# Kernel tuning notes

Measured on AMD Instinct MI355X. Metric: run time of the kernel, lower is better.

## Reference

```python
import jax, jax.numpy as jnp
import numpy as np

NUM_HEADS = 8

def setup_inputs() -> dict:
    key = jax.random.key(0)
    ks = jax.random.split(key, 8)
    B, T, J, N, C = 4, 16, 17, 17, 256
    x = jax.random.normal(ks[0], (B, T, J, N, C), dtype=jnp.float32)
    A_s = jax.random.uniform(ks[1], (J, J), dtype=jnp.float32)
    A_v = jax.random.uniform(ks[2], (N, N), dtype=jnp.float32)
    W_qkv = jax.random.normal(ks[3], (C, 5 * C), dtype=jnp.float32) * (C ** -0.5)
    W_proj = jax.random.normal(ks[4], (3 * C, C), dtype=jnp.float32) * ((3 * C) ** -0.5)
    b_proj = jnp.zeros((C,), dtype=jnp.float32)
    # M ~ xavier_uniform(gain=1.414) over shape (1, J, N, C)
    bound = 1.414 * np.sqrt(6.0 / (N + C))
    M = jax.random.uniform(ks[5], (1, J, N, C), dtype=jnp.float32, minval=-bound, maxval=bound)
    adj_s = jnp.full((J, J), 1e-6, dtype=jnp.float32)  # torch stores (1,1,J,J); broadcast-identical
    adj_v = jnp.full((N, N), 1e-6, dtype=jnp.float32)
    return {"x": x, "A_s": A_s, "A_v": A_v, "W_qkv": W_qkv, "W_proj": W_proj,
            "b_proj": b_proj, "M": M, "adj_s": adj_s, "adj_v": adj_v}


def reference(x, A_s, A_v, W_qkv, W_proj, b_proj, M, adj_s, adj_v):
    B, T, J, N, C = x.shape
    h = NUM_HEADS
    hc = C // h
    scale = hc ** -0.5
    bt = B * T
    xr = x.reshape(bt, J, N, C)
    # qkv Linear (no bias) then view(..., C, 5): channel-interleaved split
    qkv = (xr @ W_qkv).reshape(bt, J, N, C, 5)
    q, k, vs, vv, vsv = (qkv[..., i] * M for i in range(5))
    def heads(t):
        return t.reshape(bt, J, N, h, hc)
    q, k, vs, vv, vsv = map(heads, (q, k, vs, vv, vsv))
    # spatial attention over joints j (per node n), temporal/variate attention over n (per j)
    att_s_o = jnp.einsum('bjnhc,bknhc->bhnjk', q, k) * scale   # (bt,h,N,J,J)
    att_v_o = jnp.einsum('bjnhc,bjmhc->bhjnm', q, k) * scale   # (bt,h,J,N,N)
    att_s = jax.nn.softmax(att_s_o, axis=-1)
    att_v = jax.nn.softmax(att_v_o, axis=-1)
    # outer-product combine, algebraically separated:
    # x_vsv[b,j,n,:] = sum_{k,m} att_s[b,h,n,j,k] * att_v[b,h,j,n,m] * vsv[b,k,m,h,:]
    r = jnp.einsum('bhjnm,bkmhc->bhjnkc', att_v, vsv)           # (bt,h,J,N,J,hc)
    x_vsv = jnp.einsum('bhnjk,bhjnkc->bjnhc', att_s, r).reshape(bt, J, N, C)
    # adjacency-biased attentions (symmetrized learned bias + fixed adjacency)
    adjs = A_s + adj_s
    adjs = (adjs.T + adjs) * 0.5
    adjv = A_v + adj_v
    adjv = (adjv.T + adjv) * 0.5
    att_s2 = jax.nn.softmax(att_s_o + adjs, axis=-1)
    att_v2 = jax.nn.softmax(att_v_o + adjv, axis=-1)
    x_vs = jnp.einsum('bhnjk,bknhc->bjnhc', att_s2, vs).reshape(bt, J, N, C)
    x_vv = jnp.einsum('bhjnm,bjmhc->bjnhc', att_v2, vv).reshape(bt, J, N, C)
    out = jnp.concatenate([x_vsv, x_vs, x_vv], axis=-1) @ W_proj + b_proj
    return out.reshape(B, T, J, N, C)
```

## Files before the change

kernel.cpp:

```cpp
#include <hip/hip_runtime.h>
#include <math.h>

#define ROWS 18496
#define SCALE 0.17677669529663687f

typedef unsigned short ushort_t;
typedef __attribute__((ext_vector_type(8))) short short8;
typedef __attribute__((ext_vector_type(4))) float f32x4;

__device__ __forceinline__ void fma4(float4& d, float s, const float4& v) {
    d.x = fmaf(s, v.x, d.x); d.y = fmaf(s, v.y, d.y);
    d.z = fmaf(s, v.z, d.z); d.w = fmaf(s, v.w, d.w);
}
__device__ __forceinline__ float dot4(const float4& a, const float4& b) {
    return a.x*b.x + a.y*b.y + a.z*b.z + a.w*b.w;
}

__device__ __forceinline__ ushort_t f2bf(float x) {
    union { float f; unsigned u; } v; v.f = x;
    unsigned r = v.u + 0x7fffu + ((v.u >> 16) & 1u);
    return (ushort_t)(r >> 16);
}
__device__ __forceinline__ float bf2f(ushort_t b) {
    union { unsigned u; float f; } v; v.u = ((unsigned)b) << 16; return v.f;
}

__device__ __forceinline__ void gl_lds16(const void* g, void* l) {
    __builtin_amdgcn_global_load_lds(
        (const __attribute__((address_space(1))) void*)g,
        (__attribute__((address_space(3))) void*)l, 16, 0, 0);
}

__device__ __forceinline__ void store_hilo(ushort_t* yhi, ushort_t* ylo,
                                           size_t off, const float4& a)
{
    ushort4 h, l;
    h.x = f2bf(a.x); l.x = f2bf(a.x - bf2f(h.x));
    h.y = f2bf(a.y); l.y = f2bf(a.y - bf2f(h.y));
    h.z = f2bf(a.z); l.z = f2bf(a.z - bf2f(h.z));
    h.w = f2bf(a.w); l.w = f2bf(a.w - bf2f(h.w));
    *(ushort4*)&yhi[off] = h;
    *(ushort4*)&ylo[off] = l;
}

__global__ __launch_bounds__(256) void k_cvt_xw(
    const float4* __restrict__ x, ushort4* __restrict__ xhi, ushort4* __restrict__ xlo,
    const float* __restrict__ W, ushort_t* __restrict__ bh, ushort_t* __restrict__ bl)
{
    if (blockIdx.x < 4624) {
        int i = blockIdx.x * 256 + threadIdx.x;
        float4 v = x[i];
        ushort4 h, l;
        h.x = f2bf(v.x); l.x = f2bf(v.x - bf2f(h.x));
        h.y = f2bf(v.y); l.y = f2bf(v.y - bf2f(h.y));
        h.z = f2bf(v.z); l.z = f2bf(v.z - bf2f(h.z));
        h.w = f2bf(v.w); l.w = f2bf(v.w - bf2f(h.w));
        xhi[i] = h; xlo[i] = l;
    } else {
        int o = blockIdx.x - 4624;
        int kk = threadIdx.x;
        int col = (o & 255) * 5 + (o >> 8);
        float v = W[(size_t)kk * 1280 + col];
        ushort_t hh = f2bf(v);
        bh[(size_t)o * 256 + kk] = hh;
        bl[(size_t)o * 256 + kk] = f2bf(v - bf2f(hh));
    }
}

__global__ __launch_bounds__(256) void k_cvt_wp(
    const float* __restrict__ W, ushort_t* __restrict__ bh, ushort_t* __restrict__ bl)
{
    int n = blockIdx.x;
    for (int k = threadIdx.x; k < 768; k += 256) {
        float v = W[(size_t)k * 256 + n];
        ushort_t h = f2bf(v);
        bh[(size_t)n * 768 + k] = h;
        bl[(size_t)n * 768 + k] = f2bf(v - bf2f(h));
    }
}

template<int BM, int BN, int K, int MODE>
__global__ __launch_bounds__(256) void k_gemm(
    const ushort_t* __restrict__ Ahi, const ushort_t* __restrict__ Alo,
    const ushort_t* __restrict__ Bhi, const ushort_t* __restrict__ Blo,
    const float* __restrict__ aux,
    float* __restrict__ out)
{
    constexpr int MT = BM / 32;
    constexpr int NT = BN / 32;
    __shared__ __attribute__((aligned(16))) ushort_t sAh[BM * 32];
    __shared__ __attribute__((aligned(16))) ushort_t sAl[BM * 32];
    __shared__ __attribute__((aligned(16))) ushort_t sBh[BN * 32];
    __shared__ __attribute__((aligned(16))) ushort_t sBl[BN * 32];

    const int t = threadIdx.x;
    const int lane = t & 63;
    const int ln = lane & 15, quad = lane >> 4;
    const int wave = t >> 6;
    const int wm = wave >> 1, wn = wave & 1;
    const int m0 = blockIdx.y * BM, n0 = blockIdx.x * BN;

    f32x4 acc[MT][NT];
#pragma unroll
    for (int i = 0; i < MT; ++i)
#pragma unroll
        for (int j = 0; j < NT; ++j) acc[i][j] = (f32x4){0.f, 0.f, 0.f, 0.f};

    for (int kb = 0; kb < K; kb += 32) {
        __syncthreads();
#pragma unroll
        for (int s = t; s < BM * 4; s += 256) {
            int row = s >> 2, kc = s & 3;
            int gr = m0 + row; if (gr > ROWS - 1) gr = ROWS - 1;
            size_t gb = ((size_t)gr * K + kb) * 2 + kc * 16;
            int lb = (s & ~63) * 16;
            gl_lds16((const char*)Ahi + gb, (char*)sAh + lb);
            gl_lds16((const char*)Alo + gb, (char*)sAl + lb);
        }
#pragma unroll
        for (int s = t; s < BN * 4; s += 256) {
            int row = s >> 2, kc = s & 3;
            size_t gb = ((size_t)(n0 + row) * K + kb) * 2 + kc * 16;
            int lb = (s & ~63) * 16;
            gl_lds16((const char*)Bhi + gb, (char*)sBh + lb);
            gl_lds16((const char*)Blo + gb, (char*)sBl + lb);
        }
        __syncthreads();

        short8 ah[MT], al[MT], bh[NT], bl[NT];
#pragma unroll
        for (int i = 0; i < MT; ++i) {
            int off = (wm * (BM / 2) + i * 16 + ln) * 32 + quad * 8;
            ah[i] = *(const short8*)&sAh[off];
            al[i] = *(const short8*)&sAl[off];
        }
#pragma unroll
        for (int j = 0; j < NT; ++j) {
            int off = (wn * (BN / 2) + j * 16 + ln) * 32 + quad * 8;
            bh[j] = *(const short8*)&sBh[off];
            bl[j] = *(const short8*)&sBl[off];
        }
#pragma unroll
        for (int i = 0; i < MT; ++i)
#pragma unroll
            for (int j = 0; j < NT; ++j) {
                acc[i][j] = __builtin_amdgcn_mfma_f32_16x16x32_bf16(ah[i], bh[j], acc[i][j], 0, 0, 0);
                acc[i][j] = __builtin_amdgcn_mfma_f32_16x16x32_bf16(ah[i], bl[j], acc[i][j], 0, 0, 0);
                acc[i][j] = __builtin_amdgcn_mfma_f32_16x16x32_bf16(al[i], bh[j], acc[i][j], 0, 0, 0);
            }
    }

#pragma unroll
    for (int i = 0; i < MT; ++i) {
#pragma unroll
        for (int r = 0; r < 4; ++r) {
            int gm = m0 + wm * (BM / 2) + i * 16 + quad * 4 + r;
            if (gm >= ROWS) continue;
            if (MODE == 0) {
                int jn = gm % 289;
                const float* Mrow = &aux[(size_t)jn * 256];
#pragma unroll
                for (int j = 0; j < NT; ++j) {
                    int gn = n0 + wn * (BN / 2) + j * 16 + ln;
                    out[(size_t)gm * 1280 + gn] = acc[i][j][r] * Mrow[gn & 255];
                }
            } else {
#pragma unroll
                for (int j = 0; j < NT; ++j) {
                    int gn = n0 + wn * (BN / 2) + j * 16 + ln;
                    out[(size_t)gm * 256 + gn] = acc[i][j][r] + aux[gn];
                }
            }
        }
    }
}

__global__ __launch_bounds__(512) void k_att(
    const float* __restrict__ qkv5,
    const float* __restrict__ A_s, const float* __restrict__ A_v,
    const float* __restrict__ adjS, const float* __restrict__ adjV,
    ushort_t* __restrict__ yhi, ushort_t* __restrict__ ylo)
{
    __shared__ __attribute__((aligned(16))) float sm[16184];
    float* aS  = sm;
    float* aV  = sm + 4913;
    float* ebS = sm + 9826;
    float* ebV = sm + 10115;
    float* buf = sm + 10404;

    const int t  = threadIdx.x;
    const int bh = blockIdx.x;
    const int b  = bh >> 3, h = bh & 7;
    const size_t rowbase = (size_t)b * 289;

    for (int idx = t; idx < 578; idx += 512) {
        int f = idx / 289, rem = idx % 289;
        int jj = rem / 17, kk = rem % 17;
        float bias;
        if (f == 0)
            bias = 0.5f * ((A_s[jj*17+kk] + adjS[jj*17+kk]) + (A_s[kk*17+jj] + adjS[kk*17+jj]));
        else
            bias = 0.5f * ((A_v[jj*17+kk] + adjV[jj*17+kk]) + (A_v[kk*17+jj] + adjV[kk*17+jj]));
        (f ? ebV : ebS)[rem] = expf(bias);
    }

    float accA[17], accB[17];
#pragma unroll
    for (int i = 0; i < 17; ++i) { accA[i] = 0.f; accB[i] = 0.f; }
    const int u2 = t + 512;
    for (int ch = 0; ch < 2; ++ch) {
        __syncthreads();
        for (int idx = t; idx < 1156; idx += 512) {
            int p = idx >> 2, c = idx & 3;
            *(float4*)&buf[p * 20 + c * 4] =
                *(const float4*)&qkv5[(rowbase + p) * 1280 + 256 + h * 32 + ch * 16 + c * 4];
        }
        __syncthreads();
        {
            const bool isS = (t < 289);
            const int p = isS ? t : t - 289;
            const float* qp = &qkv5[(rowbase + p) * 1280 + h * 32 + ch * 16];
            float4 q0 = *(const float4*)&qp[0];
            float4 q1 = *(const float4*)&qp[4];
            float4 q2 = *(const float4*)&qp[8];
            float4 q3 = *(const float4*)&qp[12];
            const int a = p / 17, bb = p % 17;
            if (isS) {
#pragma unroll
                for (int kk = 0; kk < 17; ++kk) {
                    const float4* r = (const float4*)&buf[(kk * 17 + bb) * 20];
                    accA[kk] += dot4(q0, r[0]) + dot4(q1, r[1]) + dot4(q2, r[2]) + dot4(q3, r[3]);
                }
            } else {
#pragma unroll
                for (int mm = 0; mm < 17; ++mm) {
                    const float4* r = (const float4*)&buf[(a * 17 + mm) * 20];
                    accA[mm] += dot4(q0, r[0]) + dot4(q1, r[1]) + dot4(q2, r[2]) + dot4(q3, r[3]);
                }
            }
        }
        if (u2 < 578) {
            const int p = u2 - 289;
            const float* qp = &qkv5[(rowbase + p) * 1280 + h * 32 + ch * 16];
            float4 q0 = *(const float4*)&qp[0];
            float4 q1 = *(const float4*)&qp[4];
            float4 q2 = *(const float4*)&qp[8];
            float4 q3 = *(const float4*)&qp[12];
            const int a = p / 17;
#pragma unroll
            for (int mm = 0; mm < 17; ++mm) {
                const float4* r = (const float4*)&buf[(a * 17 + mm) * 20];
                accB[mm] += dot4(q0, r[0]) + dot4(q1, r[1]) + dot4(q2, r[2]) + dot4(q3, r[3]);
            }
        }
    }
    {
        if (t < 289) {
            const int a = t / 17, bb = t % 17;
#pragma unroll
            for (int kk = 0; kk < 17; ++kk) aS[bb * 289 + a * 17 + kk] = accA[kk] * SCALE;
        } else {
            const int p = t - 289;
            const int a = p / 17, bb = p % 17;
#pragma unroll
            for (int mm = 0; mm < 17; ++mm) aV[a * 289 + bb * 17 + mm] = accA[mm] * SCALE;
        }
        if (u2 < 578) {
            const int p = u2 - 289;
            const int a = p / 17, bb = p % 17;
#pragma unroll
            for (int mm = 0; mm < 17; ++mm) aV[a * 289 + bb * 17 + mm] = accB[mm] * SCALE;
        }
    }
    __syncthreads();

    for (int idx = t; idx < 578; idx += 512) {
        float* row = (idx < 289) ? &aS[idx * 17] : &aV[(idx - 289) * 17];
        float v[17];
#pragma unroll
        for (int kk = 0; kk < 17; ++kk) v[kk] = row[kk];
        float mx = v[0];
#pragma unroll
        for (int kk = 1; kk < 17; ++kk) mx = fmaxf(mx, v[kk]);
        float sum = 0.f;
#pragma unroll
        for (int kk = 0; kk < 17; ++kk) { v[kk] = expf(v[kk] - mx); sum += v[kk]; }
        float inv = 1.f / sum;
#pragma unroll
        for (int kk = 0; kk < 17; ++kk) row[kk] = v[kk] * inv;
    }

    for (int ch = 0; ch < 2; ++ch) {
        __syncthreads();
        for (int idx = t; idx < 1156; idx += 512) {
            int p = idx >> 2, c = idx & 3;
            *(float4*)&buf[p * 20 + c * 4] =
                *(const float4*)&qkv5[(rowbase + p) * 1280 + 1024 + h * 32 + ch * 16 + c * 4];
        }
        __syncthreads();
        for (int u = t; u < 580; u += 512) {
            const int c4 = (u & 3) * 4;
            const int pb = (u >> 2) * 2;
            const int nv = (289 - pb < 2) ? 1 : 2;
            const int p1 = (pb + 1 > 288) ? 288 : pb + 1;
            const int jj0 = pb / 17, nn0 = pb % 17;
            const int jj1 = p1 / 17, nn1 = p1 % 17;
            float eV0[17], eV1[17];
            {
                const float* s0 = &aV[jj0 * 289 + nn0 * 17];
                const float* s1 = &aV[jj1 * 289 + nn1 * 17];
#pragma unroll
                for (int m = 0; m < 17; ++m) { eV0[m] = s0[m]; eV1[m] = s1[m]; }
            }
            float4 acc0 = {0,0,0,0}, acc1 = {0,0,0,0};
            for (int kk = 0; kk < 17; ++kk) {
                float4 tg0 = {0,0,0,0}, tg1 = {0,0,0,0};
#pragma unroll
                for (int m = 0; m < 17; ++m) {
                    float4 v = *(const float4*)&buf[(kk * 17 + m) * 20 + c4];
                    fma4(tg0, eV0[m], v);
                    fma4(tg1, eV1[m], v);
                }
                fma4(acc0, aS[nn0 * 289 + jj0 * 17 + kk], tg0);
                fma4(acc1, aS[nn1 * 289 + jj1 * 17 + kk], tg1);
            }
            store_hilo(yhi, ylo, (rowbase + pb) * 768 + h * 32 + ch * 16 + c4, acc0);
            if (nv == 2)
                store_hilo(yhi, ylo, (rowbase + pb + 1) * 768 + h * 32 + ch * 16 + c4, acc1);
        }
    }

    for (int ch = 0; ch < 2; ++ch) {
        __syncthreads();
        for (int idx = t; idx < 1156; idx += 512) {
            int p = idx >> 2, c = idx & 3;
            *(float4*)&buf[p * 20 + c * 4] =
                *(const float4*)&qkv5[(rowbase + p) * 1280 + 512 + h * 32 + ch * 16 + c * 4];
        }
        __syncthreads();
        for (int u = t; u < 1156; u += 512) {
            const int c4 = (u & 3) * 4, rest = u >> 2;
            const int n = rest % 17, j = rest / 17;
            float w[17];
            float s = 0.f;
            const float* as = &aS[n * 289 + j * 17];
            const float* eb = &ebS[j * 17];
#pragma unroll
            for (int kk = 0; kk < 17; ++kk) { w[kk] = as[kk] * eb[kk]; s += w[kk]; }
            const float inv = 1.f / s;
            float4 a0 = {0,0,0,0};
            for (int kk = 0; kk < 17; ++kk) {
                float4 v = *(const float4*)&buf[(kk * 17 + n) * 20 + c4];
                fma4(a0, w[kk], v);
            }
            a0.x *= inv; a0.y *= inv; a0.z *= inv; a0.w *= inv;
            store_hilo(yhi, ylo, (rowbase + j * 17 + n) * 768 + 256 + h * 32 + ch * 16 + c4, a0);
        }
    }

    for (int ch = 0; ch < 2; ++ch) {
        __syncthreads();
        for (int idx = t; idx < 1156; idx += 512) {
            int p = idx >> 2, c = idx & 3;
            *(float4*)&buf[p * 20 + c * 4] =
                *(const float4*)&qkv5[(rowbase + p) * 1280 + 768 + h * 32 + ch * 16 + c * 4];
        }
        __syncthreads();
        for (int u = t; u < 1156; u += 512) {
            const int c4 = (u & 3) * 4, rest = u >> 2;
            const int j = rest % 17, n = rest / 17;
            float w[17];
            float s = 0.f;
            const float* av = &aV[j * 289 + n * 17];
            const float* eb = &ebV[n * 17];
#pragma unroll
            for (int mm = 0; mm < 17; ++mm) { w[mm] = av[mm] * eb[mm]; s += w[mm]; }
            const float inv = 1.f / s;
            float4 a0 = {0,0,0,0};
            for (int mm = 0; mm < 17; ++mm) {
                float4 v = *(const float4*)&buf[(j * 17 + mm) * 20 + c4];
                fma4(a0, w[mm], v);
            }
            a0.x *= inv; a0.y *= inv; a0.z *= inv; a0.w *= inv;
            store_hilo(yhi, ylo, (rowbase + j * 17 + n) * 768 + 512 + h * 32 + ch * 16 + c4, a0);
        }
    }
}

extern "C" void kernel_launch(void* const* d_in, const int* in_sizes, int n_in,
                              void* d_out, int out_size, void* d_ws, size_t ws_size,
                              hipStream_t stream)
{
    const float* x    = (const float*)d_in[0];
    const float* A_s  = (const float*)d_in[1];
    const float* A_v  = (const float*)d_in[2];
    const float* Wqkv = (const float*)d_in[3];
    const float* Wp   = (const float*)d_in[4];
    const float* bp   = (const float*)d_in[5];
    const float* M    = (const float*)d_in[6];
    const float* adjS = (const float*)d_in[7];
    const float* adjV = (const float*)d_in[8];
    float* out = (float*)d_out;

    char* w = (char*)d_ws;
    float*    qkv5  = (float*)w;
    ushort_t* wph   = (ushort_t*)w;
    ushort_t* wpl   = (ushort_t*)(w + 393216);
    char* R = w + 134946816;
    ushort_t* xhi = (ushort_t*)R;
    ushort_t* xlo = (ushort_t*)(R + 9469952);
    ushort_t* wqh = (ushort_t*)(R + 18939904);
    ushort_t* wql = (ushort_t*)(R + 19595264);
    ushort_t* yhi = (ushort_t*)R;
    ushort_t* ylo = (ushort_t*)(R + 28422144);

    k_cvt_xw<<<dim3(5904), 256, 0, stream>>>((const float4*)x, (ushort4*)xhi, (ushort4*)xlo,
                                             Wqkv, wqh, wql);
    k_gemm<128, 128, 256, 0><<<dim3(10, 145), 256, 0, stream>>>(xhi, xlo, wqh, wql, M, qkv5);
    k_att<<<dim3(512), 512, 0, stream>>>(qkv5, A_s, A_v, adjS, adjV, yhi, ylo);
    k_cvt_wp<<<dim3(256), 256, 0, stream>>>(Wp, wph, wpl);
    k_gemm<128, 64, 768, 1><<<dim3(4, 145), 256, 0, stream>>>(yhi, ylo, wph, wpl, bp, out);
}
```

Measured before the change: 309.6 us.

## Cut register pressure in attention kernel to allow two blocks per CU

Adds a minimum-blocks hint of 2 to k_att's launch bounds. The per-thread score accumulators now live in shared memory: channel 0 writes them and channel 1 adds to them, with the scale moved into the softmax. The x_vsv loop handles one output row per thread instead of two, which drops the second set of attention weights and accumulators. This is meant to raise occupancy and hide latency. The cost is extra LDS read-modify-write traffic and losing the reuse of each loaded value across two rows, so LDS reads in the 17x17 inner loop roughly double.

```diff
diff --git a/kernel.cpp b/kernel.cpp
--- a/kernel.cpp
+++ b/kernel.cpp
@@ -175,7 +175,7 @@
     }
 }
 
-__global__ __launch_bounds__(512) void k_att(
+__global__ __launch_bounds__(512, 2) void k_att(
     const float* __restrict__ qkv5,
     const float* __restrict__ A_s, const float* __restrict__ A_v,
     const float* __restrict__ adjS, const float* __restrict__ adjV,
@@ -204,10 +204,6 @@
         (f ? ebV : ebS)[rem] = expf(bias);
     }
 
-    float accA[17], accB[17];
-#pragma unroll
-    for (int i = 0; i < 17; ++i) { accA[i] = 0.f; accB[i] = 0.f; }
-    const int u2 = t + 512;
     for (int ch = 0; ch < 2; ++ch) {
         __syncthreads();
         for (int idx = t; idx < 1156; idx += 512) {
@@ -216,60 +212,45 @@
                 *(const float4*)&qkv5[(rowbase + p) * 1280 + 256 + h * 32 + ch * 16 + c * 4];
         }
         __syncthreads();
-        {
-            const bool isS = (t < 289);
-            const int p = isS ? t : t - 289;
+        for (int u = t; u < 578; u += 512) {
+            const bool isS = (u < 289);
+            const int p = isS ? u : u - 289;
             const float* qp = &qkv5[(rowbase + p) * 1280 + h * 32 + ch * 16];
             float4 q0 = *(const float4*)&qp[0];
             float4 q1 = *(const float4*)&qp[4];
             float4 q2 = *(const float4*)&qp[8];
             float4 q3 = *(const float4*)&qp[12];
             const int a = p / 17, bb = p % 17;
+            float tmp[17];
             if (isS) {
 #pragma unroll
                 for (int kk = 0; kk < 17; ++kk) {
                     const float4* r = (const float4*)&buf[(kk * 17 + bb) * 20];
-                    accA[kk] += dot4(q0, r[0]) + dot4(q1, r[1]) + dot4(q2, r[2]) + dot4(q3, r[3]);
+                    tmp[kk] = dot4(q0, r[0]) + dot4(q1, r[1]) + dot4(q2, r[2]) + dot4(q3, r[3]);
+                }
+                float* dst = &aS[bb * 289 + a * 17];
+                if (ch == 0) {
+#pragma unroll
+                    for (int kk = 0; kk < 17; ++kk) dst[kk] = tmp[kk];
+                } else {
+#pragma unroll
+                    for (int kk = 0; kk < 17; ++kk) dst[kk] += tmp[kk];
                 }
             } else {
 #pragma unroll
                 for (int mm = 0; mm < 17; ++mm) {
                     const float4* r = (const float4*)&buf[(a * 17 + mm) * 20];
-                    accA[mm] += dot4(q0, r[0]) + dot4(q1, r[1]) + dot4(q2, r[2]) + dot4(q3, r[3]);
-                }
-            }
-        }
-        if (u2 < 578) {
-            const int p = u2 - 289;
-            const float* qp = &qkv5[(rowbase + p) * 1280 + h * 32 + ch * 16];
-            float4 q0 = *(const float4*)&qp[0];
-            float4 q1 = *(const float4*)&qp[4];
-            float4 q2 = *(const float4*)&qp[8];
-            float4 q3 = *(const float4*)&qp[12];
-            const int a = p / 17;
-#pragma unroll
-            for (int mm = 0; mm < 17; ++mm) {
-                const float4* r = (const float4*)&buf[(a * 17 + mm) * 20];
-                accB[mm] += dot4(q0, r[0]) + dot4(q1, r[1]) + dot4(q2, r[2]) + dot4(q3, r[3]);
-            }
-        }
-    }
-    {
-        if (t < 289) {
-            const int a = t / 17, bb = t % 17;
-#pragma unroll
-            for (int kk = 0; kk < 17; ++kk) aS[bb * 289 + a * 17 + kk] = accA[kk] * SCALE;
-        } else {
-            const int p = t - 289;
-            const int a = p / 17, bb = p % 17;
-#pragma unroll
-            for (int mm = 0; mm < 17; ++mm) aV[a * 289 + bb * 17 + mm] = accA[mm] * SCALE;
-        }
-        if (u2 < 578) {
-            const int p = u2 - 289;
-            const int a = p / 17, bb = p % 17;
-#pragma unroll
-            for (int mm = 0; mm < 17; ++mm) aV[a * 289 + bb * 17 + mm] = accB[mm] * SCALE;
+                    tmp[mm] = dot4(q0, r[0]) + dot4(q1, r[1]) + dot4(q2, r[2]) + dot4(q3, r[3]);
+                }
+                float* dst = &aV[a * 289 + bb * 17];
+                if (ch == 0) {
+#pragma unroll
+                    for (int mm = 0; mm < 17; ++mm) dst[mm] = tmp[mm];
+                } else {
+#pragma unroll
+                    for (int mm = 0; mm < 17; ++mm) dst[mm] += tmp[mm];
+                }
+            }
         }
     }
     __syncthreads();
@@ -278,7 +259,7 @@
         float* row = (idx < 289) ? &aS[idx * 17] : &aV[(idx - 289) * 17];
         float v[17];
 #pragma unroll
-        for (int kk = 0; kk < 17; ++kk) v[kk] = row[kk];
+        for (int kk = 0; kk < 17; ++kk) v[kk] = row[kk] * SCALE;
         float mx = v[0];
 #pragma unroll
         for (int kk = 1; kk < 17; ++kk) mx = fmaxf(mx, v[kk]);
@@ -298,35 +279,27 @@
                 *(const float4*)&qkv5[(rowbase + p) * 1280 + 1024 + h * 32 + ch * 16 + c * 4];
         }
         __syncthreads();
-        for (int u = t; u < 580; u += 512) {
+        for (int u = t; u < 1156; u += 512) {
             const int c4 = (u & 3) * 4;
-            const int pb = (u >> 2) * 2;
-            const int nv = (289 - pb < 2) ? 1 : 2;
-            const int p1 = (pb + 1 > 288) ? 288 : pb + 1;
-            const int jj0 = pb / 17, nn0 = pb % 17;
-            const int jj1 = p1 / 17, nn1 = p1 % 17;
-            float eV0[17], eV1[17];
+            const int p = u >> 2;
+            const int jj = p / 17, nn = p % 17;
+            float eV[17];
             {
-                const float* s0 = &aV[jj0 * 289 + nn0 * 17];
-                const float* s1 = &aV[jj1 * 289 + nn1 * 17];
-#pragma unroll
-                for (int m = 0; m < 17; ++m) { eV0[m] = s0[m]; eV1[m] = s1[m]; }
-            }
-            float4 acc0 = {0,0,0,0}, acc1 = {0,0,0,0};
+                const float* s0 = &aV[jj * 289 + nn * 17];
+#pragma unroll
+                for (int m = 0; m < 17; ++m) eV[m] = s0[m];
+            }
+            float4 acc0 = {0,0,0,0};
             for (int kk = 0; kk < 17; ++kk) {
-                float4 tg0 = {0,0,0,0}, tg1 = {0,0,0,0};
+                float4 tg0 = {0,0,0,0};
 #pragma unroll
                 for (int m = 0; m < 17; ++m) {
                     float4 v = *(const float4*)&buf[(kk * 17 + m) * 20 + c4];
-                    fma4(tg0, eV0[m], v);
-                    fma4(tg1, eV1[m], v);
-                }
-                fma4(acc0, aS[nn0 * 289 + jj0 * 17 + kk], tg0);
-                fma4(acc1, aS[nn1 * 289 + jj1 * 17 + kk], tg1);
-            }
-            store_hilo(yhi, ylo, (rowbase + pb) * 768 + h * 32 + ch * 16 + c4, acc0);
-            if (nv == 2)
-                store_hilo(yhi, ylo, (rowbase + pb + 1) * 768 + h * 32 + ch * 16 + c4, acc1);
+                    fma4(tg0, eV[m], v);
+                }
+                fma4(acc0, aS[nn * 289 + jj * 17 + kk], tg0);
+            }
+            store_hilo(yhi, ylo, (rowbase + p) * 768 + h * 32 + ch * 16 + c4, acc0);
         }
     }
 
```

After: 309.7 us. Within noise of the previous version (+0.0%).
